# Optimization experiments

Hardware: AMD Instinct MI355X
Metric: run time of the kernel (lower is better)

## Reference

```python
import jax, jax.numpy as jnp
import numpy as np

B, C, E, HLR, WLR = 2, 64, 4, 192, 192


def setup_inputs() -> dict:
    key = jax.random.key(0)
    ks = jax.random.split(key, 8)
    s = 0.05  # keep activations/offsets in a sane range
    return {
        "x": jax.random.normal(ks[0], (B, C, HLR, WLR), jnp.float32),
        "fused": jax.random.normal(ks[1], (B, C, HLR, WLR), jnp.float32),
        "weight_compress": jax.random.normal(ks[2], (E, C // 8, C), jnp.float32) * s,
        "weight_expand": jax.random.normal(ks[3], (E, C, C // 8), jnp.float32) * s,
        "body_w1": jax.random.normal(ks[4], (64, 4), jnp.float32) * s,
        "body_b1": jnp.zeros((64,), jnp.float32),
        "body_w2": jax.random.normal(ks[5], (64, 64), jnp.float32) * s,
        "body_b2": jnp.zeros((64,), jnp.float32),
        "routing_w": jax.random.normal(ks[6], (E, 64), jnp.float32) * s,
        "routing_b": jnp.zeros((E,), jnp.float32),
        "offset_w": jax.random.normal(ks[7], (2, 64), jnp.float32) * s,
        "offset_b": jnp.zeros((2,), jnp.float32),
        "scale": 2,
    }


def _conv1x1(x, w, b):
    # x: [n, cin, H, W], w: [cout, cin] (1x1 conv)
    return jnp.einsum('oc,nchw->nohw', w, x) + b[None, :, None, None]


def _grid_sample(img, px, py):
    # Bilinear sample, align_corners=True semantics, zeros padding.
    # img: [b,c,h,w]; px, py: [b,H,W] absolute LR pixel coords.
    b, c, h, w = img.shape
    x0 = jnp.floor(px)
    y0 = jnp.floor(py)
    wx = (px - x0)[:, None]  # [b,1,H,W]
    wy = (py - y0)[:, None]

    def gather(xi, yi):
        valid = (xi >= 0) & (xi <= w - 1) & (yi >= 0) & (yi <= h - 1)
        xc = jnp.clip(xi, 0, w - 1).astype(jnp.int32)
        yc = jnp.clip(yi, 0, h - 1).astype(jnp.int32)
        v = jax.vmap(lambda im, yy, xx: im[:, yy, xx])(img, yc, xc)  # [b,c,H,W]
        return v * valid[:, None].astype(img.dtype)

    v00 = gather(x0, y0)
    v01 = gather(x0 + 1, y0)
    v10 = gather(x0, y0 + 1)
    v11 = gather(x0 + 1, y0 + 1)
    top = v00 * (1 - wx) + v01 * wx
    bot = v10 * (1 - wx) + v11 * wx
    return top * (1 - wy) + bot * wy


def reference(x, fused, weight_compress, weight_expand, body_w1, body_b1,
              body_w2, body_b2, routing_w, routing_b, offset_w, offset_b, scale):
    b, c, h, w = fused.shape
    H, W = round(h * scale), round(w * scale)
    e, c8 = weight_compress.shape[0], weight_compress.shape[1]

    ch = jnp.arange(H, dtype=jnp.float32)
    cw = jnp.arange(W, dtype=jnp.float32)
    coor_h = (ch + 0.5) / scale - jnp.floor((ch + 0.5) / scale + 0.001) - 0.5  # [H]
    coor_w = (cw + 0.5) / scale - jnp.floor((cw + 0.5) / scale + 0.001) - 0.5  # [W]
    inp = jnp.stack([
        jnp.full((H, W), 1.0 / scale, jnp.float32),
        jnp.full((H, W), 1.0 / scale, jnp.float32),
        jnp.broadcast_to(coor_h[:, None], (H, W)),
        jnp.broadcast_to(coor_w[None, :], (H, W)),
    ], 0)[None]  # [1,4,H,W]

    emb = jax.nn.relu(_conv1x1(inp, body_w1, body_b1))
    emb = jax.nn.relu(_conv1x1(emb, body_w2, body_b2))
    offset = _conv1x1(emb, offset_w, offset_b)            # [1,2,H,W]
    routing = jax.nn.sigmoid(_conv1x1(emb, routing_w, routing_b))  # [1,E,H,W]

    rw = routing.reshape(e, H * W).T                      # [HW, E]
    wc = (rw @ weight_compress.reshape(e, -1)).reshape(H, W, c8, c)  # per-pixel compress
    we = (rw @ weight_expand.reshape(e, -1)).reshape(H, W, c, c8)    # per-pixel expand

    # deformable sample: HR grid projected into LR space + learned offset (pixel units)
    px = jnp.broadcast_to((cw[None, :] + 0.5) / scale - 0.5, (H, W))[None] + offset[:, 0]
    py = jnp.broadcast_to((ch[:, None] + 0.5) / scale - 0.5, (H, W))[None] + offset[:, 1]
    px = jnp.broadcast_to(px, (b, H, W))
    py = jnp.broadcast_to(py, (b, H, W))
    fea0 = _grid_sample(fused, px, py)                    # [b,c,H,W]

    fea = fea0.transpose(0, 2, 3, 1)                      # [b,H,W,c]
    mid = jnp.einsum('hwoc,bhwc->bhwo', wc, fea)          # [b,H,W,c//8]
    out = jnp.einsum('hwco,bhwo->bhwc', we, mid)          # [b,H,W,c]
    return out.transpose(0, 3, 1, 2) + fea0
```

## Files before the change

### kernel.cpp

```cpp
#include <hip/hip_runtime.h>
#include <math.h>

typedef __attribute__((ext_vector_type(8))) short short8;
typedef __attribute__((ext_vector_type(4))) float f32x4;

#define HLR_ 192
#define WLR_ 192
#define H_ 384
#define W_ 384
#define LRP (HLR_*WLR_)
#define PTILES (LRP/64)
#define TPX 128
#define NTW (W_/TPX)

#define WS_K_OFF 4718592
#define WS_OFF_OFF (WS_K_OFF + 8192)

__device__ __forceinline__ unsigned short f32_bf16(float x){
    union { float f; unsigned int u; } v; v.f = x;
    unsigned int r = v.u + 0x7fffu + ((v.u >> 16) & 1u);
    return (unsigned short)(r >> 16);
}
__device__ __forceinline__ float bf16_f32(unsigned short h){
    union { float f; unsigned int u; } v; v.u = ((unsigned int)h) << 16;
    return v.f;
}

__global__ __launch_bounds__(256) void precompute_kernel(
    const float* __restrict__ w1, const float* __restrict__ b1,
    const float* __restrict__ w2, const float* __restrict__ b2,
    const float* __restrict__ rw, const float* __restrict__ rb,
    const float* __restrict__ ow, const float* __restrict__ ob,
    const float* __restrict__ WC, const float* __restrict__ WE,
    unsigned short* __restrict__ Kmat, float* __restrict__ g_off)
{
    __shared__ float sW2[64*65];
    __shared__ float sRW[6*64];
    __shared__ float sE1[4][64];
    __shared__ float sR[4][4];
    __shared__ float sWc[4][8][64];
    __shared__ float sWe[4][64][8];

    int tid = threadIdx.x;
    for (int idx = tid; idx < 4096; idx += 256)
        sW2[(idx>>6)*65 + (idx&63)] = w2[idx];
    if (tid < 256) sRW[tid] = rw[tid];
    if (tid < 128) sRW[256 + tid] = ow[tid];

    int wave = tid >> 6, lane = tid & 63;
    int ph = wave >> 1, pw = wave & 1;

    float ch = (ph + 0.5f)*0.5f;
    float coor_h = ch - floorf(ch + 0.001f) - 0.5f;
    float cw = (pw + 0.5f)*0.5f;
    float coor_w = cw - floorf(cw + 0.001f) - 0.5f;

    float e1 = w1[lane*4+0]*0.5f + w1[lane*4+1]*0.5f
             + w1[lane*4+2]*coor_h + w1[lane*4+3]*coor_w + b1[lane];
    sE1[wave][lane] = fmaxf(e1, 0.0f);
    __syncthreads();

    float e2 = b2[lane];
    #pragma unroll 16
    for (int i = 0; i < 64; ++i) e2 += sW2[lane*65 + i] * sE1[wave][i];
    e2 = fmaxf(e2, 0.0f);

    #pragma unroll
    for (int k = 0; k < 6; ++k) {
        float t = sRW[k*64 + lane] * e2;
        #pragma unroll
        for (int m = 1; m <= 32; m <<= 1) t += __shfl_xor(t, m, 64);
        if (lane == 0) {
            if (k < 4) sR[wave][k] = 1.0f/(1.0f + expf(-(t + rb[k])));
            else       g_off[wave*2 + (k-4)] = t + ob[k-4];
        }
    }
    __syncthreads();

    for (int idx = tid; idx < 2048; idx += 256) {
        int cls = idx >> 9, rem = idx & 511;
        float r0=sR[cls][0], r1=sR[cls][1], r2=sR[cls][2], r3=sR[cls][3];
        sWc[cls][rem>>6][rem&63] =
            r0*WC[0*512+rem] + r1*WC[1*512+rem] + r2*WC[2*512+rem] + r3*WC[3*512+rem];
    }
    for (int idx = tid; idx < 2048; idx += 256) {
        int cls = idx >> 9, rem = idx & 511;
        float r0=sR[cls][0], r1=sR[cls][1], r2=sR[cls][2], r3=sR[cls][3];
        sWe[cls][rem>>3][rem&7] =
            r0*WE[0*512+rem] + r1*WE[1*512+rem] + r2*WE[2*512+rem] + r3*WE[3*512+rem];
    }
    __syncthreads();

    for (int idx = tid; idx < 16384; idx += 256) {
        int cls = idx >> 12, rem = idx & 4095;
        int c = rem >> 6, cp = rem & 63;
        float a = 0.0f;
        #pragma unroll
        for (int o = 0; o < 8; ++o) a += sWe[cls][c][o] * sWc[cls][o][cp];
        Kmat[idx] = f32_bf16(a);
    }
}

__global__ __launch_bounds__(256) void transpose_kernel(
    const float* __restrict__ fused, float* __restrict__ fused_t)
{
    __shared__ float tile[64][65];
    int bid = blockIdx.x;
    int b = bid / PTILES, pt = bid % PTILES;
    int p0 = pt * 64;
    int tid = threadIdx.x;
    int tlo = tid & 63, thi = tid >> 6;
    #pragma unroll
    for (int i = 0; i < 16; ++i) {
        int c = thi + i*4;
        tile[c][tlo] = fused[(size_t)(b*64 + c)*LRP + p0 + tlo];
    }
    __syncthreads();
    #pragma unroll
    for (int i = 0; i < 16; ++i) {
        int p = thi + i*4;
        fused_t[(size_t)(b*LRP + p0 + p)*64 + tlo] = tile[tlo][p];
    }
}

__global__ __launch_bounds__(256, 4) void main_kernel(
    const float* __restrict__ fused_t, const unsigned short* __restrict__ Kmat,
    const float* __restrict__ g_off, float* __restrict__ out)
{
    __shared__ unsigned short sFea[256*72];

    int g = blockIdx.x;
    int xcd = g & 7;
    int t = g >> 3;
    int q = t / 3;
    int wt = t - q*3;
    int h = xcd*48 + q;
    int w0 = wt * TPX;
    int tid = threadIdx.x, wave = tid >> 6, lane = tid & 63;
    int b = wave >> 1, par = wave & 1;
    int ph = h & 1, cls = ph*2 + par;

    float off0 = g_off[cls*2 + 0];
    float off1 = g_off[cls*2 + 1];

    float py  = (h + 0.5f)*0.5f - 0.5f + off1;
    float y0f = floorf(py);
    float wy  = py - y0f;
    int   y0  = (int)y0f;
    float fy0 = (y0 >= 0  && y0 <= HLR_-1) ? 1.0f : 0.0f;
    float fy1 = (y0 >= -1 && y0 <= HLR_-2) ? 1.0f : 0.0f;
    int   yc0 = min(max(y0, 0), HLR_-1);
    int   yc1 = min(max(y0+1, 0), HLR_-1);
    float omwy = 1.0f - wy;

    float pxb  = (w0 + par + 0.5f)*0.5f - 0.5f + off0;
    float x0bf = floorf(pxb);
    float wx   = pxb - x0bf;
    int   x0b  = (int)x0bf;
    float omwx = 1.0f - wx;

    float W00 = omwx*omwy*fy0, W01 = wx*omwy*fy0;
    float W10 = omwx*wy  *fy1, W11 = wx*wy  *fy1;

    int itg = lane >> 4;
    int cg  = lane & 15;

    const float* baseB = fused_t + (size_t)b * LRP * 64;
    const float* r0 = baseB + (size_t)yc0 * WLR_ * 64 + cg*4;
    const float* r1 = baseB + (size_t)yc1 * WLR_ * 64 + cg*4;
    unsigned short* sW = sFea + wave*64*72 + cg*4;

    #pragma unroll
    for (int j = 0; j < 16; ++j) {
        int item = j*4 + itg;
        int x0 = x0b + item;
        float fx0 = (x0 >= 0  && x0 <= WLR_-1) ? 1.0f : 0.0f;
        float fx1 = (x0 >= -1 && x0 <= WLR_-2) ? 1.0f : 0.0f;
        int xc0 = min(max(x0, 0), WLR_-1);
        int xc1 = min(max(x0+1, 0), WLR_-1);
        float a00 = W00*fx0, a01 = W01*fx1, a10 = W10*fx0, a11 = W11*fx1;
        f32x4 v00 = *(const f32x4*)(r0 + (size_t)xc0*64);
        f32x4 v01 = *(const f32x4*)(r0 + (size_t)xc1*64);
        f32x4 v10 = *(const f32x4*)(r1 + (size_t)xc0*64);
        f32x4 v11 = *(const f32x4*)(r1 + (size_t)xc1*64);
        f32x4 v = v00*a00 + v01*a01 + v10*a10 + v11*a11;
        ushort4 u;
        u.x = f32_bf16(v[0]); u.y = f32_bf16(v[1]);
        u.z = f32_bf16(v[2]); u.w = f32_bf16(v[3]);
        *(ushort4*)(sW + item*72) = u;
    }
    __syncthreads();

    int lm = lane & 15, lg = lane >> 4;

    short8 Bf[2][4];
    #pragma unroll
    for (int nt = 0; nt < 4; ++nt)
        #pragma unroll
        for (int kt = 0; kt < 2; ++kt)
            Bf[kt][nt] = *(const short8*)(sFea + (wave*64 + nt*16 + lm)*72 + kt*32 + lg*8);

    const unsigned short* Kc = Kmat + cls*4096;
    short8 Af[4][2];
    #pragma unroll
    for (int mt = 0; mt < 4; ++mt)
        #pragma unroll
        for (int kt = 0; kt < 2; ++kt)
            Af[mt][kt] = *(const short8*)(Kc + (mt*16 + lm)*64 + kt*32 + lg*8);

    f32x4 acc[4][4];
    #pragma unroll
    for (int mt = 0; mt < 4; ++mt) {
        #pragma unroll
        for (int nt = 0; nt < 4; ++nt) {
            f32x4 a = {0.0f, 0.0f, 0.0f, 0.0f};
            a = __builtin_amdgcn_mfma_f32_16x16x32_bf16(Af[mt][0], Bf[0][nt], a, 0, 0, 0);
            a = __builtin_amdgcn_mfma_f32_16x16x32_bf16(Af[mt][1], Bf[1][nt], a, 0, 0, 0);
            acc[mt][nt] = a;
        }
    }

    #pragma unroll
    for (int mt = 0; mt < 4; ++mt) {
        #pragma unroll
        for (int nt = 0; nt < 4; ++nt) {
            int slot = wave*64 + nt*16 + lm;
            ushort4 idv = *(const ushort4*)(sFea + slot*72 + mt*16 + lg*4);
            int wc = w0 + 2*(nt*16 + lm) + par;
            int c0 = mt*16 + lg*4;
            float* op = out + (((size_t)(b*64 + c0)*H_ + h)*W_ + wc);
            op[0*(size_t)(H_*W_)] = acc[mt][nt][0] + bf16_f32(idv.x);
            op[1*(size_t)(H_*W_)] = acc[mt][nt][1] + bf16_f32(idv.y);
            op[2*(size_t)(H_*W_)] = acc[mt][nt][2] + bf16_f32(idv.z);
            op[3*(size_t)(H_*W_)] = acc[mt][nt][3] + bf16_f32(idv.w);
        }
    }
}

extern "C" void kernel_launch(void* const* d_in, const int* in_sizes, int n_in,
                              void* d_out, int out_size, void* d_ws, size_t ws_size,
                              hipStream_t stream)
{
    const float* fused = (const float*)d_in[1];
    const float* WC    = (const float*)d_in[2];
    const float* WE    = (const float*)d_in[3];
    const float* w1    = (const float*)d_in[4];
    const float* b1    = (const float*)d_in[5];
    const float* w2    = (const float*)d_in[6];
    const float* b2    = (const float*)d_in[7];
    const float* rw    = (const float*)d_in[8];
    const float* rb    = (const float*)d_in[9];
    const float* ow    = (const float*)d_in[10];
    const float* ob    = (const float*)d_in[11];
    (void)in_sizes; (void)n_in; (void)out_size; (void)ws_size;

    float* ws = (float*)d_ws;
    float* fused_t = ws;
    unsigned short* Kmat = (unsigned short*)(ws + WS_K_OFF);
    float* g_off = ws + WS_OFF_OFF;
    float* o = (float*)d_out;

    hipLaunchKernelGGL(precompute_kernel, dim3(1), dim3(256), 0, stream,
                       w1, b1, w2, b2, rw, rb, ow, ob, WC, WE, Kmat, g_off);
    hipLaunchKernelGGL(transpose_kernel, dim3(2*PTILES), dim3(256), 0, stream,
                       fused, fused_t);
    hipLaunchKernelGGL(main_kernel, dim3(H_*NTW), dim3(256), 0, stream,
                       fused_t, Kmat, g_off, o);
}
```

Measured before the change: 155.8 us.

## Merge precompute and transpose into one launch, fold residual into identity weights

Combines the single-block weight precompute and the fused-tensor transpose into one prep kernel, with block 0 doing the precompute and the remaining blocks doing the transpose, which saves a kernel launch and lets the two overlap. The residual add is folded into the per-class matrix by adding the identity, so the main kernel no longer re-reads the bf16 features from shared memory in its epilogue. bf16 packing now uses the paired conversion intrinsic. Folding identity into a bf16-rounded matrix changes rounding of the residual slightly.

```diff
diff --git a/kernel.cpp b/kernel.cpp
--- a/kernel.cpp
+++ b/kernel.cpp
@@ -1,4 +1,5 @@
 #include <hip/hip_runtime.h>
+#include <hip/hip_bf16.h>
 #include <math.h>
 
 typedef __attribute__((ext_vector_type(8))) short short8;
@@ -21,12 +22,15 @@
     unsigned int r = v.u + 0x7fffu + ((v.u >> 16) & 1u);
     return (unsigned short)(r >> 16);
 }
-__device__ __forceinline__ float bf16_f32(unsigned short h){
-    union { float f; unsigned int u; } v; v.u = ((unsigned int)h) << 16;
-    return v.f;
-}
-
-__global__ __launch_bounds__(256) void precompute_kernel(
+__device__ __forceinline__ unsigned int pk_bf16(float a, float b){
+    float2 t; t.x = a; t.y = b;
+    __hip_bfloat162 h = __float22bfloat162_rn(t);
+    union { __hip_bfloat162 h; unsigned int u; } c; c.h = h;
+    return c.u;
+}
+
+__global__ __launch_bounds__(256) void prep_kernel(
+    const float* __restrict__ fused, float* __restrict__ fused_t,
     const float* __restrict__ w1, const float* __restrict__ b1,
     const float* __restrict__ w2, const float* __restrict__ b2,
     const float* __restrict__ rw, const float* __restrict__ rb,
@@ -34,92 +38,93 @@
     const float* __restrict__ WC, const float* __restrict__ WE,
     unsigned short* __restrict__ Kmat, float* __restrict__ g_off)
 {
-    __shared__ float sW2[64*65];
-    __shared__ float sRW[6*64];
-    __shared__ float sE1[4][64];
-    __shared__ float sR[4][4];
-    __shared__ float sWc[4][8][64];
-    __shared__ float sWe[4][64][8];
-
+    __shared__ float smem[8912];
+    int bid = blockIdx.x;
     int tid = threadIdx.x;
-    for (int idx = tid; idx < 4096; idx += 256)
-        sW2[(idx>>6)*65 + (idx&63)] = w2[idx];
-    if (tid < 256) sRW[tid] = rw[tid];
-    if (tid < 128) sRW[256 + tid] = ow[tid];
-
-    int wave = tid >> 6, lane = tid & 63;
-    int ph = wave >> 1, pw = wave & 1;
-
-    float ch = (ph + 0.5f)*0.5f;
-    float coor_h = ch - floorf(ch + 0.001f) - 0.5f;
-    float cw = (pw + 0.5f)*0.5f;
-    float coor_w = cw - floorf(cw + 0.001f) - 0.5f;
-
-    float e1 = w1[lane*4+0]*0.5f + w1[lane*4+1]*0.5f
-             + w1[lane*4+2]*coor_h + w1[lane*4+3]*coor_w + b1[lane];
-    sE1[wave][lane] = fmaxf(e1, 0.0f);
-    __syncthreads();
-
-    float e2 = b2[lane];
-    #pragma unroll 16
-    for (int i = 0; i < 64; ++i) e2 += sW2[lane*65 + i] * sE1[wave][i];
-    e2 = fmaxf(e2, 0.0f);
-
-    #pragma unroll
-    for (int k = 0; k < 6; ++k) {
-        float t = sRW[k*64 + lane] * e2;
-        #pragma unroll
-        for (int m = 1; m <= 32; m <<= 1) t += __shfl_xor(t, m, 64);
-        if (lane == 0) {
-            if (k < 4) sR[wave][k] = 1.0f/(1.0f + expf(-(t + rb[k])));
-            else       g_off[wave*2 + (k-4)] = t + ob[k-4];
-        }
-    }
-    __syncthreads();
-
-    for (int idx = tid; idx < 2048; idx += 256) {
-        int cls = idx >> 9, rem = idx & 511;
-        float r0=sR[cls][0], r1=sR[cls][1], r2=sR[cls][2], r3=sR[cls][3];
-        sWc[cls][rem>>6][rem&63] =
-            r0*WC[0*512+rem] + r1*WC[1*512+rem] + r2*WC[2*512+rem] + r3*WC[3*512+rem];
-    }
-    for (int idx = tid; idx < 2048; idx += 256) {
-        int cls = idx >> 9, rem = idx & 511;
-        float r0=sR[cls][0], r1=sR[cls][1], r2=sR[cls][2], r3=sR[cls][3];
-        sWe[cls][rem>>3][rem&7] =
-            r0*WE[0*512+rem] + r1*WE[1*512+rem] + r2*WE[2*512+rem] + r3*WE[3*512+rem];
-    }
-    __syncthreads();
-
-    for (int idx = tid; idx < 16384; idx += 256) {
-        int cls = idx >> 12, rem = idx & 4095;
-        int c = rem >> 6, cp = rem & 63;
-        float a = 0.0f;
-        #pragma unroll
-        for (int o = 0; o < 8; ++o) a += sWe[cls][c][o] * sWc[cls][o][cp];
-        Kmat[idx] = f32_bf16(a);
-    }
-}
-
-__global__ __launch_bounds__(256) void transpose_kernel(
-    const float* __restrict__ fused, float* __restrict__ fused_t)
-{
-    __shared__ float tile[64][65];
-    int bid = blockIdx.x;
-    int b = bid / PTILES, pt = bid % PTILES;
-    int p0 = pt * 64;
-    int tid = threadIdx.x;
-    int tlo = tid & 63, thi = tid >> 6;
-    #pragma unroll
-    for (int i = 0; i < 16; ++i) {
-        int c = thi + i*4;
-        tile[c][tlo] = fused[(size_t)(b*64 + c)*LRP + p0 + tlo];
-    }
-    __syncthreads();
-    #pragma unroll
-    for (int i = 0; i < 16; ++i) {
-        int p = thi + i*4;
-        fused_t[(size_t)(b*LRP + p0 + p)*64 + tlo] = tile[tlo][p];
+
+    if (bid == 0) {
+        float* sW2 = smem;
+        float* sRW = smem + 4160;
+        float* sE1 = smem + 4544;
+        float* sR  = smem + 4800;
+        float* sWc = smem + 4816;
+        float* sWe = smem + 6864;
+
+        for (int idx = tid; idx < 4096; idx += 256)
+            sW2[(idx>>6)*65 + (idx&63)] = w2[idx];
+        sRW[tid] = rw[tid];
+        if (tid < 128) sRW[256 + tid] = ow[tid];
+
+        int wave = tid >> 6, lane = tid & 63;
+        int ph = wave >> 1, pw = wave & 1;
+
+        float ch = (ph + 0.5f)*0.5f;
+        float coor_h = ch - floorf(ch + 0.001f) - 0.5f;
+        float cw = (pw + 0.5f)*0.5f;
+        float coor_w = cw - floorf(cw + 0.001f) - 0.5f;
+
+        float e1 = w1[lane*4+0]*0.5f + w1[lane*4+1]*0.5f
+                 + w1[lane*4+2]*coor_h + w1[lane*4+3]*coor_w + b1[lane];
+        sE1[wave*64 + lane] = fmaxf(e1, 0.0f);
+        __syncthreads();
+
+        float e2 = b2[lane];
+        #pragma unroll 16
+        for (int i = 0; i < 64; ++i) e2 += sW2[lane*65 + i] * sE1[wave*64 + i];
+        e2 = fmaxf(e2, 0.0f);
+
+        #pragma unroll
+        for (int k = 0; k < 6; ++k) {
+            float t = sRW[k*64 + lane] * e2;
+            #pragma unroll
+            for (int m = 1; m <= 32; m <<= 1) t += __shfl_xor(t, m, 64);
+            if (lane == 0) {
+                if (k < 4) sR[wave*4 + k] = 1.0f/(1.0f + expf(-(t + rb[k])));
+                else       g_off[wave*2 + (k-4)] = t + ob[k-4];
+            }
+        }
+        __syncthreads();
+
+        for (int idx = tid; idx < 2048; idx += 256) {
+            int cls = idx >> 9, rem = idx & 511;
+            float r0=sR[cls*4+0], r1=sR[cls*4+1], r2=sR[cls*4+2], r3=sR[cls*4+3];
+            sWc[cls*512 + rem] =
+                r0*WC[0*512+rem] + r1*WC[1*512+rem] + r2*WC[2*512+rem] + r3*WC[3*512+rem];
+        }
+        for (int idx = tid; idx < 2048; idx += 256) {
+            int cls = idx >> 9, rem = idx & 511;
+            float r0=sR[cls*4+0], r1=sR[cls*4+1], r2=sR[cls*4+2], r3=sR[cls*4+3];
+            sWe[cls*512 + rem] =
+                r0*WE[0*512+rem] + r1*WE[1*512+rem] + r2*WE[2*512+rem] + r3*WE[3*512+rem];
+        }
+        __syncthreads();
+
+        for (int idx = tid; idx < 16384; idx += 256) {
+            int cls = idx >> 12, rem = idx & 4095;
+            int c = rem >> 6, cp = rem & 63;
+            float a = (c == cp) ? 1.0f : 0.0f;
+            #pragma unroll
+            for (int o = 0; o < 8; ++o)
+                a += sWe[cls*512 + c*8 + o] * sWc[cls*512 + o*64 + cp];
+            Kmat[idx] = f32_bf16(a);
+        }
+    } else {
+        float* tile = smem;
+        int id = bid - 1;
+        int b = id / PTILES, pt = id % PTILES;
+        int p0 = pt * 64;
+        int tlo = tid & 63, thi = tid >> 6;
+        #pragma unroll
+        for (int i = 0; i < 16; ++i) {
+            int c = thi + i*4;
+            tile[c*65 + tlo] = fused[(size_t)(b*64 + c)*LRP + p0 + tlo];
+        }
+        __syncthreads();
+        #pragma unroll
+        for (int i = 0; i < 16; ++i) {
+            int p = thi + i*4;
+            fused_t[(size_t)(b*LRP + p0 + p)*64 + tlo] = tile[tlo*65 + p];
+        }
     }
 }
 
@@ -184,10 +189,10 @@
         f32x4 v10 = *(const f32x4*)(r1 + (size_t)xc0*64);
         f32x4 v11 = *(const f32x4*)(r1 + (size_t)xc1*64);
         f32x4 v = v00*a00 + v01*a01 + v10*a10 + v11*a11;
-        ushort4 u;
-        u.x = f32_bf16(v[0]); u.y = f32_bf16(v[1]);
-        u.z = f32_bf16(v[2]); u.w = f32_bf16(v[3]);
-        *(ushort4*)(sW + item*72) = u;
+        uint2 pv;
+        pv.x = pk_bf16(v[0], v[1]);
+        pv.y = pk_bf16(v[2], v[3]);
+        *(uint2*)(sW + item*72) = pv;
     }
     __syncthreads();
 
@@ -224,15 +229,13 @@
     for (int mt = 0; mt < 4; ++mt) {
         #pragma unroll
         for (int nt = 0; nt < 4; ++nt) {
-            int slot = wave*64 + nt*16 + lm;
-            ushort4 idv = *(const ushort4*)(sFea + slot*72 + mt*16 + lg*4);
             int wc = w0 + 2*(nt*16 + lm) + par;
             int c0 = mt*16 + lg*4;
             float* op = out + (((size_t)(b*64 + c0)*H_ + h)*W_ + wc);
-            op[0*(size_t)(H_*W_)] = acc[mt][nt][0] + bf16_f32(idv.x);
-            op[1*(size_t)(H_*W_)] = acc[mt][nt][1] + bf16_f32(idv.y);
-            op[2*(size_t)(H_*W_)] = acc[mt][nt][2] + bf16_f32(idv.z);
-            op[3*(size_t)(H_*W_)] = acc[mt][nt][3] + bf16_f32(idv.w);
+            op[0*(size_t)(H_*W_)] = acc[mt][nt][0];
+            op[1*(size_t)(H_*W_)] = acc[mt][nt][1];
+            op[2*(size_t)(H_*W_)] = acc[mt][nt][2];
+            op[3*(size_t)(H_*W_)] = acc[mt][nt][3];
         }
     }
 }
@@ -260,10 +263,9 @@
     float* g_off = ws + WS_OFF_OFF;
     float* o = (float*)d_out;
 
-    hipLaunchKernelGGL(precompute_kernel, dim3(1), dim3(256), 0, stream,
-                       w1, b1, w2, b2, rw, rb, ow, ob, WC, WE, Kmat, g_off);
-    hipLaunchKernelGGL(transpose_kernel, dim3(2*PTILES), dim3(256), 0, stream,
-                       fused, fused_t);
+    hipLaunchKernelGGL(prep_kernel, dim3(1 + 2*PTILES), dim3(256), 0, stream,
+                       fused, fused_t, w1, b1, w2, b2, rw, rb, ow, ob, WC, WE,
+                       Kmat, g_off);
     hipLaunchKernelGGL(main_kernel, dim3(H_*NTW), dim3(256), 0, stream,
                        fused_t, Kmat, g_off, o);
 }
```

Result: faster. 150.5 us (-3.4%).
